# Kernel tuning notes

Measured on AMD Instinct MI355X. Metric: run time of the kernel, lower is better.

The kernel has to match this reference:

```python
import jax, jax.numpy as jnp
import numpy as np

B, N, D, H = 8, 1024, 1024, 16
HD = D // H  # head_size = 64


def setup_inputs() -> dict:
    key = jax.random.key(0)
    k0, k1, k2, k3, k4 = jax.random.split(key, 5)
    scale = 1.0 / np.sqrt(D)
    return {
        "x": jax.random.normal(k0, (B, N, D), dtype=jnp.float32),
        "Wqkv": jax.random.normal(k1, (D, 3 * D), dtype=jnp.float32) * scale,
        "bqkv": jnp.zeros((3 * D,), dtype=jnp.float32),
        "Wo": jax.random.normal(k2, (D, D), dtype=jnp.float32) * scale,
        "bo": jnp.zeros((D,), dtype=jnp.float32),
    }


def reference(x, Wqkv, bqkv, Wo, bo):
    # Fused QKV projection: [B, N, 3D]
    qkv = jnp.einsum("bnd,de->bne", x, Wqkv) + bqkv
    q, k, v = jnp.split(qkv, 3, axis=-1)

    def split_heads(t):  # [B, N, D] -> [B, H, N, HD]
        return t.reshape(B, N, H, HD).transpose(0, 2, 1, 3)

    q, k, v = split_heads(q), split_heads(k), split_heads(v)

    # Scaled dot-product attention (no mask, dropout=0)
    scores = jnp.einsum("bhqd,bhkd->bhqk", q, k) / jnp.sqrt(jnp.float32(HD))
    alpha = jax.nn.softmax(scores, axis=-1)
    ctx = jnp.einsum("bhqk,bhkd->bhqd", alpha, v)  # [B, H, N, HD]

    ctx = ctx.transpose(0, 2, 1, 3).reshape(B, N, D)
    out = jnp.einsum("bnd,de->bne", ctx, Wo) + bo
    return out
```

## Files before the change

### kernel.cpp

```cpp
#include <hip/hip_runtime.h>
#include <cstdint>
#include <cstddef>

typedef _Float16 half_t;
typedef __attribute__((ext_vector_type(4))) _Float16 half4v;
typedef __attribute__((ext_vector_type(8))) _Float16 half8v;
typedef __attribute__((ext_vector_type(4))) float float4v;
typedef __attribute__((ext_vector_type(16))) float float16v;
typedef __attribute__((ext_vector_type(4))) unsigned uint4v;
typedef __attribute__((ext_vector_type(2))) int int2v;

typedef __attribute__((address_space(1))) const void gv_t;
typedef __attribute__((address_space(3))) void lv_t;

__device__ __forceinline__ void lds_cp16(const void* g, void* l) {
  __builtin_amdgcn_global_load_lds((gv_t*)g, (lv_t*)l, 16, 0, 0);
}

__device__ __forceinline__ unsigned pkh(float a, float b) {
  return __builtin_bit_cast(unsigned, __builtin_amdgcn_cvt_pkrtz(a, b));
}

__global__ __launch_bounds__(256) void k_cvt(const float* __restrict__ in,
                                             half_t* __restrict__ out) {
  int i = blockIdx.x * 256 + threadIdx.x;
  float4 v = ((const float4*)in)[i];
  half4v h = {(half_t)v.x, (half_t)v.y, (half_t)v.z, (half_t)v.w};
  ((half4v*)out)[i] = h;
}

__global__ __launch_bounds__(256) void k_tcvt(const float* __restrict__ in,
                                              half_t* __restrict__ out, int R, int C) {
  __shared__ float t[32][33];
  int c0 = blockIdx.x * 32, r0 = blockIdx.y * 32;
  int tc = threadIdx.x & 31, tr = threadIdx.x >> 5;
#pragma unroll
  for (int i = 0; i < 4; i++)
    t[tr + i * 8][tc] = in[(size_t)(r0 + tr + i * 8) * C + c0 + tc];
  __syncthreads();
#pragma unroll
  for (int i = 0; i < 4; i++)
    out[(size_t)(c0 + tr + i * 8) * R + r0 + tc] = (half_t)t[tc][tr + i * 8];
}

template <int EPI>
__global__ __launch_bounds__(256, 3) void k_gemm(
    const half_t* __restrict__ A, const half_t* __restrict__ Bt,
    const float* __restrict__ bias, float* __restrict__ Cout,
    half_t* __restrict__ Qo, half_t* __restrict__ Ko, half_t* __restrict__ Vo,
    int M, int N, int K) {
  __shared__ half_t As[3][128 * 32];
  __shared__ half_t Bs[3][128 * 32];
  const int tid = threadIdx.x;
  const int lane = tid & 63;
  const int w = tid >> 6;
  const int xcd = blockIdx.x & 7;
  const int l = blockIdx.x >> 3;
  const int nc = l >> 6, r = l & 63;
  const int m0 = (xcd * 8 + (r >> 3)) * 128;
  const int n0 = (nc * 8 + (r & 7)) * 128;
  const int wr = w >> 1, wc = w & 1;

  const int c0 = w * 2, c1 = c0 + 1;
  const int srow = lane >> 2;
  const int sr0 = c0 * 16 + srow;
  const int sr1 = c1 * 16 + srow;
  const int scol = ((lane & 3) ^ ((lane >> 3) & 3)) * 8;

  const half_t* Ag0 = A + (size_t)(m0 + sr0) * K + scol;
  const half_t* Ag1 = A + (size_t)(m0 + sr1) * K + scol;
  const half_t* Bg0 = Bt + (size_t)(n0 + sr0) * K + scol;
  const half_t* Bg1 = Bt + (size_t)(n0 + sr1) * K + scol;

  float4v acc[4][4] = {};

  const int fr = lane & 15;
  const int fg = lane >> 4;
  const int cswz = (fg ^ ((fr >> 1) & 3)) * 8;
  const int aoff = (wr * 64 + fr) * 32 + cswz;
  const int boff = (wc * 64 + fr) * 32 + cswz;

  const int NT = K >> 5;
#pragma unroll
  for (int p = 0; p < 2; ++p) {
    const int kn = p * 32;
    lds_cp16(Ag0 + kn, &As[p][c0 * 512]);
    lds_cp16(Ag1 + kn, &As[p][c1 * 512]);
    lds_cp16(Bg0 + kn, &Bs[p][c0 * 512]);
    lds_cp16(Bg1 + kn, &Bs[p][c1 * 512]);
  }

  int cur = 0;
  for (int t = 0; t < NT; t++) {
    if (t + 1 < NT)
      asm volatile("s_waitcnt vmcnt(4)" ::: "memory");
    else
      asm volatile("s_waitcnt vmcnt(0)" ::: "memory");
    __builtin_amdgcn_s_barrier();
    __builtin_amdgcn_sched_barrier(0);

    if (t + 2 < NT) {
      int b2 = cur + 2;
      if (b2 >= 3) b2 -= 3;
      const int kn = (t + 2) * 32;
      lds_cp16(Ag0 + kn, &As[b2][c0 * 512]);
      lds_cp16(Ag1 + kn, &As[b2][c1 * 512]);
      lds_cp16(Bg0 + kn, &Bs[b2][c0 * 512]);
      lds_cp16(Bg1 + kn, &Bs[b2][c1 * 512]);
    }

    half8v a[4], b[4];
#pragma unroll
    for (int m = 0; m < 4; m++) a[m] = *(const half8v*)(&As[cur][aoff + m * 512]);
#pragma unroll
    for (int n = 0; n < 4; n++) b[n] = *(const half8v*)(&Bs[cur][boff + n * 512]);
    __builtin_amdgcn_s_setprio(1);
#pragma unroll
    for (int m = 0; m < 4; m++)
#pragma unroll
      for (int n = 0; n < 4; n++)
        acc[m][n] = __builtin_amdgcn_mfma_f32_16x16x32_f16(a[m], b[n], acc[m][n], 0, 0, 0);
    __builtin_amdgcn_s_setprio(0);
    cur = (cur >= 2) ? 0 : cur + 1;
  }

  const int rq = (lane >> 4) * 4;
  const int cc = lane & 15;
  if constexpr (EPI == 0) {
#pragma unroll
    for (int n = 0; n < 4; n++) {
      int e = n0 + wc * 64 + n * 16 + cc;
      float bv = bias[e];
      int which = e >> 10, h = (e >> 6) & 15, hd = e & 63;
#pragma unroll
      for (int m = 0; m < 4; m++) {
        int rowb = m0 + wr * 64 + m * 16 + rq;
#pragma unroll
        for (int r2 = 0; r2 < 4; r2++) {
          int row = rowb + r2;
          int b_ = row >> 10, tok = row & 1023;
          half_t hv = (half_t)(acc[m][n][r2] + bv);
          size_t bh = (size_t)(b_ * 16 + h);
          if (which == 0)
            Qo[(bh * 1024 + tok) * 64 + hd] = hv;
          else if (which == 1)
            Ko[(bh * 1024 + tok) * 64 + hd] = hv;
          else
            Vo[(bh * 64 + hd) * 1024 + tok] = hv;
        }
      }
    }
  } else {
#pragma unroll
    for (int n = 0; n < 4; n++) {
      int e = n0 + wc * 64 + n * 16 + cc;
      float bv = bias[e];
#pragma unroll
      for (int m = 0; m < 4; m++) {
        int rowb = m0 + wr * 64 + m * 16 + rq;
#pragma unroll
        for (int r2 = 0; r2 < 4; r2++)
          Cout[(size_t)(rowb + r2) * N + e] = acc[m][n][r2] + bv;
      }
    }
  }
}

__global__ __launch_bounds__(512, 4) void k_attn(const half_t* __restrict__ Qh,
                                                 const half_t* __restrict__ Kh,
                                                 const half_t* __restrict__ Vt,
                                                 half_t* __restrict__ ctx) {
  __shared__ alignas(16) half_t Ks[2][64 * 64];
  __shared__ alignas(16) half_t Vs[2][64 * 64];
  const int lane = threadIdx.x & 63;
  const int w = threadIdx.x >> 6;
  const int ql = lane & 31, hi = lane >> 5;
  const int xcd = blockIdx.x & 7, loc = blockIdx.x >> 3;
  const int bh = xcd * 16 + (loc >> 2), qb = loc & 3;
  const int b_ = bh >> 4, h = bh & 15;
  const int q0 = qb * 256 + w * 32;

  const half_t* Qp = Qh + (size_t)bh * (1024 * 64);
  const half_t* Kp = Kh + (size_t)bh * (1024 * 64);
  const half_t* Vp = Vt + (size_t)bh * (64 * 1024);

  half8v qf[4];
#pragma unroll
  for (int c = 0; c < 4; c++) {
    half8v tq = *(const half8v*)(Qp + (size_t)(q0 + ql) * 64 + c * 16 + hi * 8);
    qf[c] = tq * (_Float16)0.125f;
  }

  const int G = w * 64 + lane;
  const int rS = G >> 3;
  const int gS = (G & 7) ^ (rS & 7);

  float16v co[2] = {};
  float mr = -1e30f, ssum = 0.f;

  lds_cp16(Kp + (size_t)rS * 64 + gS * 8, &Ks[0][w * 512]);
  lds_cp16(Vp + (size_t)rS * 1024 + 0 + gS * 8, &Vs[0][w * 512]);
  __syncthreads();

  int cur = 0;
  for (int t = 0; t < 16; t++) {
    if (t < 15) {
      const int kn = (t + 1) * 64;
      lds_cp16(Kp + (size_t)(kn + rS) * 64 + gS * 8, &Ks[cur ^ 1][w * 512]);
      lds_cp16(Vp + (size_t)rS * 1024 + kn + gS * 8, &Vs[cur ^ 1][w * 512]);
    }

    float16v sacc[2] = {};
    __builtin_amdgcn_s_setprio(1);
#pragma unroll
    for (int c = 0; c < 4; c++)
#pragma unroll
      for (int s = 0; s < 2; s++) {
        int row = s * 32 + ql;
        half8v kf = *(const half8v*)(&Ks[cur][row * 64 + (((2 * c + hi) ^ (row & 7)) * 8)]);
        sacc[s] = __builtin_amdgcn_mfma_f32_32x32x16_f16(kf, qf[c], sacc[s], 0, 0, 0);
      }
    __builtin_amdgcn_s_setprio(0);

    float mx = -1e30f;
#pragma unroll
    for (int s = 0; s < 2; s++)
#pragma unroll
      for (int i = 0; i < 16; i++) mx = fmaxf(mx, sacc[s][i]);
    mx = fmaxf(mx, __shfl_xor(mx, 32, 64));
    if (mx > mr + 8.f) {
      float fac = __expf(mr - mx);
      mr = mx;
      ssum *= fac;
#pragma unroll
      for (int dd = 0; dd < 2; dd++)
#pragma unroll
        for (int i = 0; i < 16; i++) co[dd][i] *= fac;
    }
    float rsum = 0.f;
#pragma unroll
    for (int s = 0; s < 2; s++)
#pragma unroll
      for (int i = 0; i < 16; i++) {
        float e = __expf(sacc[s][i] - mr);
        sacc[s][i] = e;
        rsum += e;
      }
    rsum += __shfl_xor(rsum, 32, 64);
    ssum += rsum;

#pragma unroll
    for (int kc = 0; kc < 4; kc++) {
      const int s = kc >> 1, o = (kc & 1) * 8;
      unsigned dA0 = pkh(sacc[s][o + 0], sacc[s][o + 1]);
      unsigned dA1 = pkh(sacc[s][o + 2], sacc[s][o + 3]);
      unsigned dB0 = pkh(sacc[s][o + 4], sacc[s][o + 5]);
      unsigned dB1 = pkh(sacc[s][o + 6], sacc[s][o + 7]);
      int2v r0 = __builtin_amdgcn_permlane32_swap((int)dA0, (int)dB0, false, false);
      int2v r1 = __builtin_amdgcn_permlane32_swap((int)dA1, (int)dB1, false, false);
      uint4v pw = {(unsigned)r0.x, (unsigned)r1.x, (unsigned)r0.y, (unsigned)r1.y};
      half8v pf = __builtin_bit_cast(half8v, pw);
      __builtin_amdgcn_s_setprio(1);
#pragma unroll
      for (int dd = 0; dd < 2; dd++) {
        int row = dd * 32 + ql;
        half8v vf = *(const half8v*)(&Vs[cur][row * 64 + (((2 * kc + hi) ^ (row & 7)) * 8)]);
        co[dd] = __builtin_amdgcn_mfma_f32_32x32x16_f16(vf, pf, co[dd], 0, 0, 0);
      }
      __builtin_amdgcn_s_setprio(0);
    }
    __syncthreads();
    cur ^= 1;
  }

  float rinv = 1.0f / ssum;
  half_t* outp = ctx + ((size_t)(b_ * 1024 + q0 + ql) * 1024 + h * 64);
#pragma unroll
  for (int dd = 0; dd < 2; dd++)
#pragma unroll
    for (int g = 0; g < 4; g++) {
      int d0 = dd * 32 + g * 8 + hi * 4;
      unsigned p0 = pkh(co[dd][g * 4 + 0] * rinv, co[dd][g * 4 + 1] * rinv);
      unsigned p1 = pkh(co[dd][g * 4 + 2] * rinv, co[dd][g * 4 + 3] * rinv);
      *(unsigned*)(outp + d0) = p0;
      *(unsigned*)(outp + d0 + 2) = p1;
    }
}

extern "C" void kernel_launch(void* const* d_in, const int* in_sizes, int n_in,
                              void* d_out, int out_size, void* d_ws, size_t ws_size,
                              hipStream_t stream) {
  const float* x = (const float*)d_in[0];
  const float* Wqkv = (const float*)d_in[1];
  const float* bqkv = (const float*)d_in[2];
  const float* Wo = (const float*)d_in[3];
  const float* bo = (const float*)d_in[4];
  float* out = (float*)d_out;
  char* ws = (char*)d_ws;

  const size_t NEED = 75497472;
  if (ws_size < NEED) return;
  half_t* xh = (half_t*)(ws);
  half_t* wqkvT = (half_t*)(ws + 16777216);
  half_t* woT = (half_t*)(ws + 23068672);
  half_t* Qh = (half_t*)(ws + 25165824);
  half_t* Kh = (half_t*)(ws + 41943040);
  half_t* Vt = (half_t*)(ws + 58720256);
  half_t* ctxh = xh;

  k_cvt<<<8192, 256, 0, stream>>>(x, xh);
  k_tcvt<<<dim3(96, 32), 256, 0, stream>>>(Wqkv, wqkvT, 1024, 3072);
  k_tcvt<<<dim3(32, 32), 256, 0, stream>>>(Wo, woT, 1024, 1024);
  k_gemm<0><<<1536, 256, 0, stream>>>(xh, wqkvT, bqkv, nullptr, Qh, Kh, Vt,
                                      8192, 3072, 1024);
  k_attn<<<512, 512, 0, stream>>>(Qh, Kh, Vt, ctxh);
  k_gemm<1><<<512, 256, 0, stream>>>(ctxh, woT, bo, out, nullptr, nullptr, nullptr,
                                     8192, 1024, 1024);
}
```

Measured before the change: 177.8 us.

## Use dedicated 128x256-tile, 512-thread QKV GEMM kernel with double buffering

Splits the templated GEMM into a dedicated QKV projection kernel and an output-projection kernel. The QKV kernel uses 8 waves per block over a 128x256 output tile, so each A tile is reused across twice as many columns. It also switches from triple to double buffering with a full vmcnt wait each step. The aim is to cut global/LDS traffic per FLOP and the block count. The risk is less latency hiding from the shallower pipeline and the full wait per iteration.

```diff
diff --git a/kernel.cpp b/kernel.cpp
--- a/kernel.cpp
+++ b/kernel.cpp
@@ -43,12 +43,94 @@
     out[(size_t)(c0 + tr + i * 8) * R + r0 + tc] = (half_t)t[tc][tr + i * 8];
 }
 
-template <int EPI>
-__global__ __launch_bounds__(256, 3) void k_gemm(
+__global__ __launch_bounds__(512, 4) void k_qkv(
     const half_t* __restrict__ A, const half_t* __restrict__ Bt,
-    const float* __restrict__ bias, float* __restrict__ Cout,
-    half_t* __restrict__ Qo, half_t* __restrict__ Ko, half_t* __restrict__ Vo,
-    int M, int N, int K) {
+    const float* __restrict__ bias,
+    half_t* __restrict__ Qo, half_t* __restrict__ Ko, half_t* __restrict__ Vo) {
+  __shared__ half_t As[2][128 * 32];
+  __shared__ half_t Bs[2][256 * 32];
+  const int tid = threadIdx.x;
+  const int lane = tid & 63;
+  const int w = tid >> 6;
+  const int wr = w >> 2, wc = w & 3;
+  const int fr = lane & 15, fg = lane >> 4;
+
+  const int xcd = blockIdx.x & 7, l = blockIdx.x >> 3;
+  const int mi = xcd * 8 + (l & 7);
+  const int ni = l >> 3;
+  const int m0 = mi * 128, n0 = ni * 256;
+
+  const int rA = tid >> 2, sA = tid & 3;
+  const int gg = sA ^ ((rA >> 1) & 3);
+  const half_t* Agp = A + (size_t)(m0 + rA) * 1024 + gg * 8;
+  const half_t* Bgp0 = Bt + (size_t)(n0 + rA) * 1024 + gg * 8;
+  const half_t* Bgp1 = Bt + (size_t)(n0 + rA + 128) * 1024 + gg * 8;
+
+  float4v acc[4][4] = {};
+  const int cswz = (fg ^ ((fr >> 1) & 3)) * 8;
+  const int aoff = (wr * 64 + fr) * 32 + cswz;
+  const int boff = (wc * 64 + fr) * 32 + cswz;
+
+  lds_cp16(Agp, &As[0][tid * 8]);
+  lds_cp16(Bgp0, &Bs[0][tid * 8]);
+  lds_cp16(Bgp1, &Bs[0][(tid + 512) * 8]);
+
+  const int NT = 32;
+  for (int t = 0; t < NT; t++) {
+    asm volatile("s_waitcnt vmcnt(0)" ::: "memory");
+    __builtin_amdgcn_s_barrier();
+    __builtin_amdgcn_sched_barrier(0);
+    const int cb = t & 1;
+    if (t + 1 < NT) {
+      const int kn = (t + 1) * 32;
+      lds_cp16(Agp + kn, &As[cb ^ 1][tid * 8]);
+      lds_cp16(Bgp0 + kn, &Bs[cb ^ 1][tid * 8]);
+      lds_cp16(Bgp1 + kn, &Bs[cb ^ 1][(tid + 512) * 8]);
+    }
+    half8v a[4], b[4];
+#pragma unroll
+    for (int m = 0; m < 4; m++) a[m] = *(const half8v*)(&As[cb][aoff + m * 512]);
+#pragma unroll
+    for (int n = 0; n < 4; n++) b[n] = *(const half8v*)(&Bs[cb][boff + n * 512]);
+    __builtin_amdgcn_s_setprio(1);
+#pragma unroll
+    for (int m = 0; m < 4; m++)
+#pragma unroll
+      for (int n = 0; n < 4; n++)
+        acc[m][n] = __builtin_amdgcn_mfma_f32_16x16x32_f16(a[m], b[n], acc[m][n], 0, 0, 0);
+    __builtin_amdgcn_s_setprio(0);
+  }
+
+  const int rq = (lane >> 4) * 4;
+  const int cc = lane & 15;
+#pragma unroll
+  for (int n = 0; n < 4; n++) {
+    const int e = n0 + wc * 64 + n * 16 + cc;
+    const float bv = bias[e];
+    const int which = e >> 10, h = (e >> 6) & 15, hd = e & 63;
+#pragma unroll
+    for (int m = 0; m < 4; m++) {
+      const int rowb = m0 + wr * 64 + m * 16 + rq;
+#pragma unroll
+      for (int r2 = 0; r2 < 4; r2++) {
+        const int row = rowb + r2;
+        const int b_ = row >> 10, tok = row & 1023;
+        const half_t hv = (half_t)(acc[m][n][r2] + bv);
+        const size_t bh = (size_t)(b_ * 16 + h);
+        if (which == 0)
+          Qo[(bh * 1024 + tok) * 64 + hd] = hv;
+        else if (which == 1)
+          Ko[(bh * 1024 + tok) * 64 + hd] = hv;
+        else
+          Vo[(bh * 64 + hd) * 1024 + tok] = hv;
+      }
+    }
+  }
+}
+
+__global__ __launch_bounds__(256, 3) void k_gemm_o(
+    const half_t* __restrict__ A, const half_t* __restrict__ Bt,
+    const float* __restrict__ bias, float* __restrict__ Cout, int N, int K) {
   __shared__ half_t As[3][128 * 32];
   __shared__ half_t Bs[3][128 * 32];
   const int tid = threadIdx.x;
@@ -126,42 +208,16 @@
 
   const int rq = (lane >> 4) * 4;
   const int cc = lane & 15;
-  if constexpr (EPI == 0) {
-#pragma unroll
-    for (int n = 0; n < 4; n++) {
-      int e = n0 + wc * 64 + n * 16 + cc;
-      float bv = bias[e];
-      int which = e >> 10, h = (e >> 6) & 15, hd = e & 63;
-#pragma unroll
-      for (int m = 0; m < 4; m++) {
-        int rowb = m0 + wr * 64 + m * 16 + rq;
-#pragma unroll
-        for (int r2 = 0; r2 < 4; r2++) {
-          int row = rowb + r2;
-          int b_ = row >> 10, tok = row & 1023;
-          half_t hv = (half_t)(acc[m][n][r2] + bv);
-          size_t bh = (size_t)(b_ * 16 + h);
-          if (which == 0)
-            Qo[(bh * 1024 + tok) * 64 + hd] = hv;
-          else if (which == 1)
-            Ko[(bh * 1024 + tok) * 64 + hd] = hv;
-          else
-            Vo[(bh * 64 + hd) * 1024 + tok] = hv;
-        }
-      }
-    }
-  } else {
-#pragma unroll
-    for (int n = 0; n < 4; n++) {
-      int e = n0 + wc * 64 + n * 16 + cc;
-      float bv = bias[e];
-#pragma unroll
-      for (int m = 0; m < 4; m++) {
-        int rowb = m0 + wr * 64 + m * 16 + rq;
-#pragma unroll
-        for (int r2 = 0; r2 < 4; r2++)
-          Cout[(size_t)(rowb + r2) * N + e] = acc[m][n][r2] + bv;
-      }
+#pragma unroll
+  for (int n = 0; n < 4; n++) {
+    int e = n0 + wc * 64 + n * 16 + cc;
+    float bv = bias[e];
+#pragma unroll
+    for (int m = 0; m < 4; m++) {
+      int rowb = m0 + wr * 64 + m * 16 + rq;
+#pragma unroll
+      for (int r2 = 0; r2 < 4; r2++)
+        Cout[(size_t)(rowb + r2) * N + e] = acc[m][n][r2] + bv;
     }
   }
 }
@@ -311,9 +367,7 @@
   k_cvt<<<8192, 256, 0, stream>>>(x, xh);
   k_tcvt<<<dim3(96, 32), 256, 0, stream>>>(Wqkv, wqkvT, 1024, 3072);
   k_tcvt<<<dim3(32, 32), 256, 0, stream>>>(Wo, woT, 1024, 1024);
-  k_gemm<0><<<1536, 256, 0, stream>>>(xh, wqkvT, bqkv, nullptr, Qh, Kh, Vt,
-                                      8192, 3072, 1024);
+  k_qkv<<<768, 512, 0, stream>>>(xh, wqkvT, bqkv, Qh, Kh, Vt);
   k_attn<<<512, 512, 0, stream>>>(Qh, Kh, Vt, ctxh);
-  k_gemm<1><<<512, 256, 0, stream>>>(ctxh, woT, bo, out, nullptr, nullptr, nullptr,
-                                     8192, 1024, 1024);
-}
+  k_gemm_o<<<512, 256, 0, stream>>>(ctxh, woT, bo, out, 1024, 1024);
+}
```

New measurement: 180.7 us. No clear change (+1.6%).

## Switch GEMM to BK=64 double buffering with 8-chunk XOR swizzle

Applied to the files above, without the earlier changes.

Restructures the GEMM main loop from a three-stage pipeline with a K-tile of 32 to a two-stage pipeline with a K-tile of 64. Each thread now issues four async global-to-LDS copies per operand per stage, and LDS uses an 8-way XOR swizzle. The goal is fewer barriers and fewer loop iterations per unit of MFMA work. The trade-offs are doubled LDS per buffer (64KB total), a lower occupancy hint (2 blocks), and a full vmcnt(0) wait each iteration, which reduces how much load latency is hidden.

```diff
diff --git a/kernel.cpp b/kernel.cpp
--- a/kernel.cpp
+++ b/kernel.cpp
@@ -44,13 +44,13 @@
 }
 
 template <int EPI>
-__global__ __launch_bounds__(256, 3) void k_gemm(
+__global__ __launch_bounds__(256, 2) void k_gemm(
     const half_t* __restrict__ A, const half_t* __restrict__ Bt,
     const float* __restrict__ bias, float* __restrict__ Cout,
     half_t* __restrict__ Qo, half_t* __restrict__ Ko, half_t* __restrict__ Vo,
     int M, int N, int K) {
-  __shared__ half_t As[3][128 * 32];
-  __shared__ half_t Bs[3][128 * 32];
+  __shared__ half_t As[2][128 * 64];
+  __shared__ half_t Bs[2][128 * 64];
   const int tid = threadIdx.x;
   const int lane = tid & 63;
   const int w = tid >> 6;
@@ -61,67 +61,69 @@
   const int n0 = (nc * 8 + (r & 7)) * 128;
   const int wr = w >> 1, wc = w & 1;
 
-  const int c0 = w * 2, c1 = c0 + 1;
-  const int srow = lane >> 2;
-  const int sr0 = c0 * 16 + srow;
-  const int sr1 = c1 * 16 + srow;
-  const int scol = ((lane & 3) ^ ((lane >> 3) & 3)) * 8;
-
-  const half_t* Ag0 = A + (size_t)(m0 + sr0) * K + scol;
-  const half_t* Ag1 = A + (size_t)(m0 + sr1) * K + scol;
-  const half_t* Bg0 = Bt + (size_t)(n0 + sr0) * K + scol;
-  const half_t* Bg1 = Bt + (size_t)(n0 + sr1) * K + scol;
+  int sr[4];
+  int sg[4];
+#pragma unroll
+  for (int j = 0; j < 4; ++j) {
+    const int G = j * 256 + tid;
+    sr[j] = G >> 3;
+    sg[j] = (G & 7) ^ (sr[j] & 7);
+  }
 
   float4v acc[4][4] = {};
 
   const int fr = lane & 15;
   const int fg = lane >> 4;
-  const int cswz = (fg ^ ((fr >> 1) & 3)) * 8;
-  const int aoff = (wr * 64 + fr) * 32 + cswz;
-  const int boff = (wc * 64 + fr) * 32 + cswz;
-
-  const int NT = K >> 5;
-#pragma unroll
-  for (int p = 0; p < 2; ++p) {
-    const int kn = p * 32;
-    lds_cp16(Ag0 + kn, &As[p][c0 * 512]);
-    lds_cp16(Ag1 + kn, &As[p][c1 * 512]);
-    lds_cp16(Bg0 + kn, &Bs[p][c0 * 512]);
-    lds_cp16(Bg1 + kn, &Bs[p][c1 * 512]);
-  }
-
-  int cur = 0;
+  const int so0 = ((0 << 2) | fg) ^ (fr & 7);
+  const int so1 = ((1 << 2) | fg) ^ (fr & 7);
+  const int arow = wr * 64 + fr;
+  const int brow = wc * 64 + fr;
+
+  const int NT = K >> 6;
+#pragma unroll
+  for (int j = 0; j < 4; ++j) {
+    lds_cp16(A + (size_t)(m0 + sr[j]) * K + sg[j] * 8, &As[0][(j * 256 + tid) * 8]);
+    lds_cp16(Bt + (size_t)(n0 + sr[j]) * K + sg[j] * 8, &Bs[0][(j * 256 + tid) * 8]);
+  }
+
   for (int t = 0; t < NT; t++) {
-    if (t + 1 < NT)
-      asm volatile("s_waitcnt vmcnt(4)" ::: "memory");
-    else
-      asm volatile("s_waitcnt vmcnt(0)" ::: "memory");
+    asm volatile("s_waitcnt vmcnt(0)" ::: "memory");
     __builtin_amdgcn_s_barrier();
     __builtin_amdgcn_sched_barrier(0);
-
-    if (t + 2 < NT) {
-      int b2 = cur + 2;
-      if (b2 >= 3) b2 -= 3;
-      const int kn = (t + 2) * 32;
-      lds_cp16(Ag0 + kn, &As[b2][c0 * 512]);
-      lds_cp16(Ag1 + kn, &As[b2][c1 * 512]);
-      lds_cp16(Bg0 + kn, &Bs[b2][c0 * 512]);
-      lds_cp16(Bg1 + kn, &Bs[b2][c1 * 512]);
-    }
-
-    half8v a[4], b[4];
-#pragma unroll
-    for (int m = 0; m < 4; m++) a[m] = *(const half8v*)(&As[cur][aoff + m * 512]);
-#pragma unroll
-    for (int n = 0; n < 4; n++) b[n] = *(const half8v*)(&Bs[cur][boff + n * 512]);
+    const int cb = t & 1;
+    if (t + 1 < NT) {
+      const int kn = (t + 1) * 64;
+#pragma unroll
+      for (int j = 0; j < 4; ++j) {
+        lds_cp16(A + (size_t)(m0 + sr[j]) * K + kn + sg[j] * 8,
+                 &As[cb ^ 1][(j * 256 + tid) * 8]);
+        lds_cp16(Bt + (size_t)(n0 + sr[j]) * K + kn + sg[j] * 8,
+                 &Bs[cb ^ 1][(j * 256 + tid) * 8]);
+      }
+    }
+    half8v a[4][2], b[4][2];
+#pragma unroll
+    for (int m = 0; m < 4; m++) {
+      const int row = (arow + m * 16) * 64;
+      a[m][0] = *(const half8v*)(&As[cb][row + so0 * 8]);
+      a[m][1] = *(const half8v*)(&As[cb][row + so1 * 8]);
+    }
+#pragma unroll
+    for (int n = 0; n < 4; n++) {
+      const int row = (brow + n * 16) * 64;
+      b[n][0] = *(const half8v*)(&Bs[cb][row + so0 * 8]);
+      b[n][1] = *(const half8v*)(&Bs[cb][row + so1 * 8]);
+    }
     __builtin_amdgcn_s_setprio(1);
 #pragma unroll
-    for (int m = 0; m < 4; m++)
-#pragma unroll
-      for (int n = 0; n < 4; n++)
-        acc[m][n] = __builtin_amdgcn_mfma_f32_16x16x32_f16(a[m], b[n], acc[m][n], 0, 0, 0);
+    for (int kk = 0; kk < 2; kk++)
+#pragma unroll
+      for (int m = 0; m < 4; m++)
+#pragma unroll
+        for (int n = 0; n < 4; n++)
+          acc[m][n] = __builtin_amdgcn_mfma_f32_16x16x32_f16(a[m][kk], b[n][kk],
+                                                             acc[m][n], 0, 0, 0);
     __builtin_amdgcn_s_setprio(0);
-    cur = (cur >= 2) ? 0 : cur + 1;
   }
 
   const int rq = (lane >> 4) * 4;
```

Result: faster. 171.3 us (-3.7%).
